# Performance work log

Hardware: AMD Instinct MI355X
Metric: run time of the kernel (lower is better)

The kernel has to match this reference:

```python
import jax, jax.numpy as jnp
import numpy as np

B, FRAMES, IMG, PATCH = 2, 4, 224, 16
D_MODEL, D_INNER, D_STATE, DT_RANK, DEPTH, D_CONV = 256, 512, 16, 16, 12, 4
NPATCH = (IMG // PATCH) ** 2  # 196


def setup_inputs() -> dict:
    keys = iter(jax.random.split(jax.random.key(0), 80))

    def n(shape, s=0.02):
        return jax.random.normal(next(keys), shape, dtype=jnp.float32) * s

    A_init = jnp.broadcast_to(jnp.log(jnp.arange(1, D_STATE + 1, dtype=jnp.float32)), (DEPTH, D_INNER, D_STATE))
    inp = {
        'x': jax.random.normal(next(keys), (B, 3, FRAMES, IMG, IMG), dtype=jnp.float32),
        'patch_w': n((D_MODEL, 3, 1, PATCH, PATCH)),
        'patch_b': jnp.zeros((D_MODEL,), jnp.float32),
        'pos_embed': n((1, NPATCH, D_MODEL)),
        'temp_pos': n((1, FRAMES, D_MODEL)),
        'in_proj_w': n((DEPTH, 2 * D_INNER, D_MODEL), D_MODEL ** -0.5),
        'convf_w': n((DEPTH, D_INNER, D_CONV), 0.3),
        'convf_b': jnp.zeros((DEPTH, D_INNER), jnp.float32),
        'xprojf_w': n((DEPTH, DT_RANK + 2 * D_STATE, D_INNER), D_INNER ** -0.5),
        'dtf_w': n((DEPTH, D_INNER, DT_RANK), DT_RANK ** -0.5),
        'dtf_b': jnp.full((DEPTH, D_INNER), -4.6, jnp.float32) + n((DEPTH, D_INNER), 0.1),
        'A_logf': A_init,
        'Dsf': jnp.ones((DEPTH, D_INNER), jnp.float32),
        'convb_w': n((DEPTH, D_INNER, D_CONV), 0.3),
        'convb_b': jnp.zeros((DEPTH, D_INNER), jnp.float32),
        'xprojb_w': n((DEPTH, DT_RANK + 2 * D_STATE, D_INNER), D_INNER ** -0.5),
        'dtb_w': n((DEPTH, D_INNER, DT_RANK), DT_RANK ** -0.5),
        'dtb_b': jnp.full((DEPTH, D_INNER), -4.6, jnp.float32) + n((DEPTH, D_INNER), 0.1),
        'A_logb': A_init,
        'Dsb': jnp.ones((DEPTH, D_INNER), jnp.float32),
        'out_proj_w': n((DEPTH, D_MODEL, D_INNER), D_INNER ** -0.5),
        'norm_w': jnp.ones((DEPTH, D_MODEL), jnp.float32),
        'normf_w': jnp.ones((D_MODEL,), jnp.float32),
        'bbox_w1': n((D_MODEL, D_MODEL), D_MODEL ** -0.5),
        'bbox_b1': jnp.zeros((D_MODEL,), jnp.float32),
        'bbox_w2': n((3, D_MODEL), D_MODEL ** -0.5),
        'bbox_b2': jnp.zeros((3,), jnp.float32),
        'pix_w1': n((4, D_MODEL, D_MODEL), D_MODEL ** -0.5),
        'pix_b1': jnp.zeros((4, D_MODEL), jnp.float32),
        'pix_w2': n((4, 2, D_MODEL), D_MODEL ** -0.5),
        'pix_b2': jnp.zeros((4, 2), jnp.float32),
    }
    return inp


def rmsnorm(x, w, eps=1e-5):
    x = x.astype(jnp.float32)
    return x * jax.lax.rsqrt(jnp.mean(x * x, axis=-1, keepdims=True) + eps) * w


def ssm_scan(u, dt, A, Bm, Cm):
    # u, dt: [B,L,di]; Bm, Cm: [B,L,st]; A: [di,st]
    def step(h, inp):
        dt_t, B_t, C_t, u_t = inp  # [B,di],[B,st],[B,st],[B,di]
        h = jnp.exp(dt_t[..., None] * A) * h + (dt_t * u_t)[..., None] * B_t[:, None, :]
        return h, jnp.einsum('bds,bs->bd', h, C_t)
    h0 = jnp.zeros((u.shape[0], u.shape[2], A.shape[1]), u.dtype)
    xs = (dt.swapaxes(0, 1), Bm.swapaxes(0, 1), Cm.swapaxes(0, 1), u.swapaxes(0, 1))
    _, ys = jax.lax.scan(step, h0, xs)
    return ys.swapaxes(0, 1)  # [B,L,di]


def mamba_dir(x, z, cw, cb, xpw, dtw, dtb, A_log, Ds):
    L = x.shape[1]
    xp = jnp.pad(x, ((0, 0), (D_CONV - 1, 0), (0, 0)))  # causal depthwise conv
    xc = cb + sum(xp[:, k:k + L, :] * cw[:, k] for k in range(D_CONV))
    xs = jax.nn.silu(xc)
    dbl = xs @ xpw.T  # [B,L,dt_rank+2*st]
    dt = jax.nn.softplus(dbl[..., :DT_RANK] @ dtw.T + dtb)
    Bm = dbl[..., DT_RANK:DT_RANK + D_STATE]
    Cm = dbl[..., DT_RANK + D_STATE:]
    y = ssm_scan(xs, dt, -jnp.exp(A_log), Bm, Cm) + Ds * xs
    return y * jax.nn.silu(z)


def _forward(x, patch_w, patch_b, pos_embed, temp_pos, in_proj_w, convf_w, convf_b, xprojf_w, dtf_w, dtf_b, A_logf, Dsf, convb_w, convb_b, xprojb_w, dtb_w, dtb_b, A_logb, Dsb, out_proj_w, norm_w, normf_w, bbox_w1, bbox_b1, bbox_w2, bbox_b2, pix_w1, pix_b1, pix_w2, pix_b2):
    feat = jax.lax.conv_general_dilated(x, patch_w, (1, PATCH, PATCH), 'VALID', dimension_numbers=('NCDHW', 'OIDHW', 'NCDHW'))
    feat = feat + patch_b[None, :, None, None, None]
    b, c, t, h, w = feat.shape
    np_ = h * w
    tok = feat.transpose(0, 2, 3, 4, 1).reshape(b * t, np_, c) + pos_embed
    tok = tok.reshape(b, t, np_, c).transpose(0, 2, 1, 3).reshape(b * np_, t, c) + temp_pos
    tok = tok.reshape(b, np_, t, c).transpose(0, 2, 1, 3).reshape(b, t * np_, c)
    hidden, residual = tok, None
    for i in range(DEPTH):
        residual = hidden if residual is None else hidden + residual  # fused add+norm (prenorm)
        hidden = rmsnorm(residual, norm_w[i])
        xz = hidden @ in_proj_w[i].T
        xi, zi = jnp.split(xz, 2, axis=-1)
        yf = mamba_dir(xi, zi, convf_w[i], convf_b[i], xprojf_w[i], dtf_w[i], dtf_b[i], A_logf[i], Dsf[i])
        yb = mamba_dir(xi[:, ::-1], zi[:, ::-1], convb_w[i], convb_b[i], xprojb_w[i], dtb_w[i], dtb_b[i], A_logb[i], Dsb[i])[:, ::-1]
        hidden = (yf + yb) @ out_proj_w[i].T
    residual = hidden + residual
    hidden = rmsnorm(residual, normf_w)
    fus = hidden[:, :5, :]  # [B,5,hidden_dim] fusion_output for DETR head
    bbox = jax.nn.relu(fus[:, 0] @ bbox_w1.T + bbox_b1) @ bbox_w2.T + bbox_b2  # [B,3]
    pix = jnp.stack([jax.nn.sigmoid(jax.nn.relu(fus[:, i + 1] @ pix_w1[i].T + pix_b1[i]) @ pix_w2[i].T + pix_b2[i]) for i in range(4)], axis=1)  # [B,4,2]
    return jnp.concatenate([bbox, pix.reshape(bbox.shape[0], 8)], axis=-1)  # [B,11]


def reference(x, patch_w, patch_b, pos_embed, temp_pos, in_proj_w, convf_w, convf_b, xprojf_w, dtf_w, dtf_b, A_logf, Dsf, convb_w, convb_b, xprojb_w, dtb_w, dtb_b, A_logb, Dsb, out_proj_w, norm_w, normf_w, bbox_w1, bbox_b1, bbox_w2, bbox_b2, pix_w1, pix_b1, pix_w2, pix_b2):
    return _forward(x, patch_w, patch_b, pos_embed, temp_pos, in_proj_w, convf_w, convf_b, xprojf_w, dtf_w, dtf_b, A_logf, Dsf, convb_w, convb_b, xprojb_w, dtb_w, dtb_b, A_logb, Dsb, out_proj_w, norm_w, normf_w, bbox_w1, bbox_b1, bbox_w2, bbox_b2, pix_w1, pix_b1, pix_w2, pix_b2)
```

## Files before the change

### kernel.cpp

```cpp
#include <hip/hip_runtime.h>
#include <hip/hip_bf16.h>
#include <cmath>

#define BB 2
#define TT 4
#define NPATCH 196
#define LL 784
#define CC 256
#define DI 512
#define NSTATE 16
#define DEPTH 12
#define NCHUNK 49
#define CLEN 16

typedef short short8 __attribute__((ext_vector_type(8)));
typedef float f32x4 __attribute__((ext_vector_type(4)));

__device__ __forceinline__ float sigmoidf_(float x){ return 1.f/(1.f+__expf(-x)); }
__device__ __forceinline__ float siluf_(float x){ return x/(1.f+__expf(-x)); }
__device__ __forceinline__ float softplusf_(float x){ return x > 20.f ? x : log1pf(__expf(x)); }
__device__ __forceinline__ unsigned short f2bf(float f){
  union { float f; unsigned int u; } v; v.f = f;
  unsigned int u = v.u;
  return (unsigned short)((u + 0x7FFFu + ((u>>16)&1u)) >> 16);
}

__global__ void k_cvt(const float* __restrict__ src, unsigned short* __restrict__ dst, int n4)
{
  int i = blockIdx.x*256 + threadIdx.x;
  if (i < n4) {
    float4 v = *(const float4*)(src + (size_t)i*4);
    unsigned short o[4] = { f2bf(v.x), f2bf(v.y), f2bf(v.z), f2bf(v.w) };
    *(uint2*)(dst + (size_t)i*4) = *(uint2*)o;
  }
}

__global__ void k_prep_xp(const float* __restrict__ xpf, const float* __restrict__ xpb,
                          unsigned short* __restrict__ Wxp)
{
  int blk = blockIdx.x;
  int r = blk & 63; int ld = blk >> 6;
  int layer = ld >> 1, dir = ld & 1;
  const float* src = dir ? xpb : xpf;
  for (int kk = threadIdx.x; kk < 512; kk += 256) {
    float v = (r < 48) ? src[((size_t)layer*48 + r)*512 + kk] : 0.f;
    Wxp[((size_t)blk)*512 + kk] = f2bf(v);
  }
}
__global__ void k_prep_dt(const float* __restrict__ dtwf, const float* __restrict__ dtwb,
                          unsigned short* __restrict__ Wdt)
{
  int idx = blockIdx.x*256 + threadIdx.x;
  int col = idx & 31; int rest = idx >> 5;
  int d = rest & 511; int ld = rest >> 9;
  int layer = ld >> 1, dir = ld & 1;
  const float* src = dir ? dtwb : dtwf;
  float v = (col < 16) ? src[((size_t)layer*512 + d)*16 + col] : 0.f;
  Wdt[idx] = f2bf(v);
}

__global__ void k_prebias(const float* __restrict__ pb, const float* __restrict__ pos,
                          const float* __restrict__ tpos, float* __restrict__ PB)
{
  int tp = blockIdx.x;
  int t = tp / NPATCH, p = tp - t*NPATCH;
  int c = threadIdx.x;
  PB[(size_t)tp*CC + c] = pb[c] + pos[(size_t)p*CC + c] + tpos[(size_t)t*CC + c];
}

__global__ void k_im2col(const float* __restrict__ x, unsigned short* __restrict__ XCol)
{
  int row = blockIdx.x, ci = blockIdx.y;
  int b = row / LL, rem = row - b*LL;
  int t = rem / NPATCH, p = rem - t*NPATCH;
  int ph = p / 14, pc = p - ph*14;
  int ii = threadIdx.x >> 4, jj = threadIdx.x & 15;
  float v = x[(((size_t)(b*3+ci)*TT + t)*224 + (ph*16+ii))*224 + (pc*16+jj)];
  XCol[(size_t)row*768 + ci*256 + threadIdx.x] = f2bf(v);
}

__global__ __launch_bounds__(256) void k_gemm_mfma(
    const unsigned short* __restrict__ Ab,
    const float* __restrict__ Af, const float* __restrict__ Af2,
    const unsigned short* __restrict__ Wb, float* __restrict__ Out,
    const float* __restrict__ bias, int M, int Nn, int K)
{
  __shared__ short As[64][40];
  __shared__ short Bs[64][40];
  int bm = blockIdx.x*64, bn = blockIdx.y*64;
  int tid = threadIdx.x;
  int wave = tid>>6, lane = tid&63;
  int wm = (wave>>1)*32, wn = (wave&1)*32;
  int quad = lane>>4, l16 = lane&15;
  f32x4 acc[2][2];
  #pragma unroll
  for (int i=0;i<2;i++)
    #pragma unroll
    for (int j=0;j<2;j++){ acc[i][j][0]=0.f; acc[i][j][1]=0.f; acc[i][j][2]=0.f; acc[i][j][3]=0.f; }
  int sr = tid>>2, sc = (tid&3)<<3;
  int gr = bm + sr;
  for (int k0 = 0; k0 < K; k0 += 32) {
    short8 av = {0,0,0,0,0,0,0,0};
    if (gr < M) {
      if (Ab) {
        av = *(const short8*)(Ab + (size_t)gr*K + k0 + sc);
      } else {
        float4 f0 = *(const float4*)(Af + (size_t)gr*K + k0 + sc);
        float4 f1 = *(const float4*)(Af + (size_t)gr*K + k0 + sc + 4);
        if (Af2) {
          float4 g0 = *(const float4*)(Af2 + (size_t)gr*K + k0 + sc);
          float4 g1 = *(const float4*)(Af2 + (size_t)gr*K + k0 + sc + 4);
          f0.x+=g0.x; f0.y+=g0.y; f0.z+=g0.z; f0.w+=g0.w;
          f1.x+=g1.x; f1.y+=g1.y; f1.z+=g1.z; f1.w+=g1.w;
        }
        av[0]=(short)f2bf(f0.x); av[1]=(short)f2bf(f0.y); av[2]=(short)f2bf(f0.z); av[3]=(short)f2bf(f0.w);
        av[4]=(short)f2bf(f1.x); av[5]=(short)f2bf(f1.y); av[6]=(short)f2bf(f1.z); av[7]=(short)f2bf(f1.w);
      }
    }
    *(short8*)&As[sr][sc] = av;
    short8 bv = *(const short8*)(Wb + (size_t)(bn+sr)*K + k0 + sc);
    *(short8*)&Bs[sr][sc] = bv;
    __syncthreads();
    short8 a0 = *(const short8*)&As[wm    +l16][quad<<3];
    short8 a1 = *(const short8*)&As[wm+16+l16][quad<<3];
    short8 b0 = *(const short8*)&Bs[wn    +l16][quad<<3];
    short8 b1 = *(const short8*)&Bs[wn+16+l16][quad<<3];
    acc[0][0] = __builtin_amdgcn_mfma_f32_16x16x32_bf16(a0,b0,acc[0][0],0,0,0);
    acc[0][1] = __builtin_amdgcn_mfma_f32_16x16x32_bf16(a0,b1,acc[0][1],0,0,0);
    acc[1][0] = __builtin_amdgcn_mfma_f32_16x16x32_bf16(a1,b0,acc[1][0],0,0,0);
    acc[1][1] = __builtin_amdgcn_mfma_f32_16x16x32_bf16(a1,b1,acc[1][1],0,0,0);
    __syncthreads();
  }
  #pragma unroll
  for (int i=0;i<2;i++){
    #pragma unroll
    for (int r=0;r<4;r++){
      int row = bm + wm + i*16 + quad*4 + r;
      if (row < M) {
        #pragma unroll
        for (int j=0;j<2;j++){
          int col = bn + wn + j*16 + l16;
          float vv = acc[i][j][r];
          if (bias) vv += bias[(size_t)(row % LL)*Nn + col];
          Out[(size_t)row*Nn + col] = vv;
        }
      }
    }
  }
}

__global__ __launch_bounds__(256) void k_gemm_xp(
    const unsigned short* __restrict__ XSb, const unsigned short* __restrict__ Wxp,
    float* __restrict__ DBL, unsigned short* __restrict__ DBLb)
{
  __shared__ short As[64][40];
  __shared__ short Bs[64][40];
  int z = blockIdx.z;
  int bm = blockIdx.x*64;
  const unsigned short* A = XSb + (size_t)z*2*LL*DI;
  const unsigned short* W = Wxp + (size_t)z*64*DI;
  int tid = threadIdx.x;
  int wave = tid>>6, lane = tid&63;
  int wm = (wave>>1)*32, wn = (wave&1)*32;
  int quad = lane>>4, l16 = lane&15;
  f32x4 acc[2][2];
  #pragma unroll
  for (int i=0;i<2;i++)
    #pragma unroll
    for (int j=0;j<2;j++){ acc[i][j][0]=0.f; acc[i][j][1]=0.f; acc[i][j][2]=0.f; acc[i][j][3]=0.f; }
  int sr = tid>>2, sc = (tid&3)<<3;
  int gr = bm + sr;
  for (int k0 = 0; k0 < DI; k0 += 32) {
    short8 av = {0,0,0,0,0,0,0,0};
    if (gr < 2*LL) av = *(const short8*)(A + (size_t)gr*DI + k0 + sc);
    *(short8*)&As[sr][sc] = av;
    *(short8*)&Bs[sr][sc] = *(const short8*)(W + (size_t)sr*DI + k0 + sc);
    __syncthreads();
    short8 a0 = *(const short8*)&As[wm    +l16][quad<<3];
    short8 a1 = *(const short8*)&As[wm+16+l16][quad<<3];
    short8 b0 = *(const short8*)&Bs[wn    +l16][quad<<3];
    short8 b1 = *(const short8*)&Bs[wn+16+l16][quad<<3];
    acc[0][0] = __builtin_amdgcn_mfma_f32_16x16x32_bf16(a0,b0,acc[0][0],0,0,0);
    acc[0][1] = __builtin_amdgcn_mfma_f32_16x16x32_bf16(a0,b1,acc[0][1],0,0,0);
    acc[1][0] = __builtin_amdgcn_mfma_f32_16x16x32_bf16(a1,b0,acc[1][0],0,0,0);
    acc[1][1] = __builtin_amdgcn_mfma_f32_16x16x32_bf16(a1,b1,acc[1][1],0,0,0);
    __syncthreads();
  }
  #pragma unroll
  for (int i=0;i<2;i++){
    #pragma unroll
    for (int r=0;r<4;r++){
      int row = bm + wm + i*16 + quad*4 + r;
      if (row < 2*LL) {
        size_t grow = (size_t)z*2*LL + row;
        #pragma unroll
        for (int j=0;j<2;j++){
          int col = wn + j*16 + l16;
          float vv = acc[i][j][r];
          DBL[grow*64 + col] = vv;
          if (col < 32) DBLb[grow*32 + col] = (col < 16) ? f2bf(vv) : (unsigned short)0;
        }
      }
    }
  }
}

__global__ __launch_bounds__(256) void k_gemm_dt(
    const unsigned short* __restrict__ DBLb, const unsigned short* __restrict__ Wdt,
    const float* __restrict__ dtbf, const float* __restrict__ dtbb,
    float* __restrict__ DTs)
{
  __shared__ short As[64][40];
  __shared__ short Bs[64][40];
  int z = blockIdx.z;
  int bm = blockIdx.x*64, bn = blockIdx.y*64;
  const unsigned short* A = DBLb + (size_t)z*2*LL*32;
  const unsigned short* W = Wdt + (size_t)z*DI*32;
  const float* dtb = z ? dtbb : dtbf;
  int tid = threadIdx.x;
  int wave = tid>>6, lane = tid&63;
  int wm = (wave>>1)*32, wn = (wave&1)*32;
  int quad = lane>>4, l16 = lane&15;
  f32x4 acc[2][2];
  #pragma unroll
  for (int i=0;i<2;i++)
    #pragma unroll
    for (int j=0;j<2;j++){ acc[i][j][0]=0.f; acc[i][j][1]=0.f; acc[i][j][2]=0.f; acc[i][j][3]=0.f; }
  int sr = tid>>2, sc = (tid&3)<<3;
  int gr = bm + sr;
  {
    short8 av = {0,0,0,0,0,0,0,0};
    if (gr < 2*LL) av = *(const short8*)(A + (size_t)gr*32 + sc);
    *(short8*)&As[sr][sc] = av;
    *(short8*)&Bs[sr][sc] = *(const short8*)(W + (size_t)(bn+sr)*32 + sc);
    __syncthreads();
    short8 a0 = *(const short8*)&As[wm    +l16][quad<<3];
    short8 a1 = *(const short8*)&As[wm+16+l16][quad<<3];
    short8 b0 = *(const short8*)&Bs[wn    +l16][quad<<3];
    short8 b1 = *(const short8*)&Bs[wn+16+l16][quad<<3];
    acc[0][0] = __builtin_amdgcn_mfma_f32_16x16x32_bf16(a0,b0,acc[0][0],0,0,0);
    acc[0][1] = __builtin_amdgcn_mfma_f32_16x16x32_bf16(a0,b1,acc[0][1],0,0,0);
    acc[1][0] = __builtin_amdgcn_mfma_f32_16x16x32_bf16(a1,b0,acc[1][0],0,0,0);
    acc[1][1] = __builtin_amdgcn_mfma_f32_16x16x32_bf16(a1,b1,acc[1][1],0,0,0);
  }
  #pragma unroll
  for (int i=0;i<2;i++){
    #pragma unroll
    for (int r=0;r<4;r++){
      int row = bm + wm + i*16 + quad*4 + r;
      if (row < 2*LL) {
        size_t grow = (size_t)z*2*LL + row;
        #pragma unroll
        for (int j=0;j<2;j++){
          int col = bn + wn + j*16 + l16;
          DTs[grow*DI + col] = softplusf_(acc[i][j][r] + dtb[col]);
        }
      }
    }
  }
}

__global__ void k_conv_silu(const float* __restrict__ XZ,
    const float* __restrict__ cwf, const float* __restrict__ cbf,
    const float* __restrict__ cwb, const float* __restrict__ cbb,
    float* __restrict__ XSf, unsigned short* __restrict__ XSb)
{
  int dir = blockIdx.z;
  int row = blockIdx.x;
  int b = row / LL, tau = row - b*LL;
  const float* cw = dir ? cwb : cwf;
  const float* cb = dir ? cbb : cbf;
  int d = threadIdx.x;
  float4 w4 = *(const float4*)(cw + (size_t)d*4);
  float acc = cb[d];
  const float wr[4] = {w4.x, w4.y, w4.z, w4.w};
  #pragma unroll
  for (int k=0;k<4;k++){
    int tt = tau - 3 + k;
    if (tt >= 0) {
      int torig = dir ? (LL-1-tt) : tt;
      acc = fmaf(XZ[((size_t)b*LL + torig)*1024 + d], wr[k], acc);
    }
  }
  float xs = siluf_(acc);
  size_t rowbase = (size_t)(dir*BB + b)*LL + tau;
  XSf[rowbase*DI + d] = xs;
  XSb[rowbase*DI + d] = f2bf(xs);
}

__global__ void k_res_rms(const float* __restrict__ Hin, float* __restrict__ R,
                          unsigned short* __restrict__ Nout, const float* __restrict__ w, int first)
{
  int row = blockIdx.x, c = threadIdx.x;
  size_t idx = (size_t)row*CC + c;
  float h = Hin[idx];
  float r = first ? h : (h + R[idx]);
  R[idx] = r;
  float v = r*r;
  #pragma unroll
  for (int m=1;m<64;m<<=1) v += __shfl_xor(v,m);
  __shared__ float sred[4];
  if ((c & 63)==0) sred[c>>6]=v;
  __syncthreads();
  float tot = sred[0]+sred[1]+sred[2]+sred[3];
  float sc = rsqrtf(tot*(1.f/CC) + 1e-5f);
  Nout[idx] = f2bf(r*sc*w[c]);
}

__global__ void k_scan1(const float* __restrict__ XS, const float* __restrict__ DBL,
                        const float* __restrict__ DTs,
                        const float* __restrict__ Alf, const float* __restrict__ Alb,
                        float* __restrict__ Pb, float* __restrict__ Hcb)
{
  int chunk = blockIdx.x;
  int d = blockIdx.y*256 + threadIdx.x;
  int dirb = blockIdx.z;
  int dir = dirb >> 1;
  const float* Al = dir ? Alb : Alf;
  float a2[NSTATE];
  {
    const float4* ar = (const float4*)(Al + (size_t)d*NSTATE);
    #pragma unroll
    for (int q=0;q<4;q++){
      float4 v = ar[q];
      a2[q*4+0] = -__expf(v.x)*1.44269504f;
      a2[q*4+1] = -__expf(v.y)*1.44269504f;
      a2[q*4+2] = -__expf(v.z)*1.44269504f;
      a2[q*4+3] = -__expf(v.w)*1.44269504f;
    }
  }
  __shared__ float Bl[CLEN][NSTATE];
  {
    int t = threadIdx.x >> 4, s = threadIdx.x & 15;
    size_t row = ((size_t)dirb*LL + chunk*CLEN + t)*64;
    Bl[t][s] = DBL[row + 16 + s];
  }
  __syncthreads();
  size_t base = (size_t)dirb*LL*DI;
  const float* xs  = XS  + base + (size_t)chunk*CLEN*DI + d;
  const float* dtp = DTs + base + (size_t)chunk*CLEN*DI + d;
  float P[NSTATE], h[NSTATE];
  #pragma unroll
  for (int s=0;s<NSTATE;s++){ P[s]=1.f; h[s]=0.f; }
  for (int i = 0; i < CLEN; ++i) {
    float dt = dtp[(size_t)i*DI];
    float u  = xs[(size_t)i*DI];
    float du = dt*u;
    #pragma unroll
    for (int s=0;s<NSTATE;s++){
      float e = exp2f(dt*a2[s]);
      P[s] *= e;
      h[s] = fmaf(e, h[s], du*Bl[i][s]);
    }
  }
  size_t ob = ((size_t)dirb*NCHUNK + chunk)*NSTATE*DI + d;
  #pragma unroll
  for (int s=0;s<NSTATE;s++){
    Pb [ob + (size_t)s*DI] = P[s];
    Hcb[ob + (size_t)s*DI] = h[s];
  }
}

__global__ void k_scan2(const float* __restrict__ Pb, float* __restrict__ Hcb)
{
  int i = blockIdx.x*256 + threadIdx.x;
  int dirb = blockIdx.y;
  float h = 0.f;
  for (int c = 0; c < NCHUNK; ++c) {
    size_t idx = ((size_t)dirb*NCHUNK + c)*NSTATE*DI + i;
    float p = Pb[idx], hl = Hcb[idx];
    Hcb[idx] = h;
    h = fmaf(p, h, hl);
  }
}

__global__ void k_scan3(const float* __restrict__ XS, const float* __restrict__ DBL,
                        const float* __restrict__ DTs, const float* __restrict__ XZ,
                        const float* __restrict__ Alf, const float* __restrict__ Alb,
                        const float* __restrict__ Dsfp, const float* __restrict__ Dsbp,
                        const float* __restrict__ Hcb, float* __restrict__ Y)
{
  int chunk = blockIdx.x;
  int d = blockIdx.y*256 + threadIdx.x;
  int dirb = blockIdx.z;
  int dir = dirb >> 1, b = dirb & 1;
  const float* Al = dir ? Alb : Alf;
  float a2[NSTATE];
  {
    const float4* ar = (const float4*)(Al + (size_t)d*NSTATE);
    #pragma unroll
    for (int q=0;q<4;q++){
      float4 v = ar[q];
      a2[q*4+0] = -__expf(v.x)*1.44269504f;
      a2[q*4+1] = -__expf(v.y)*1.44269504f;
      a2[q*4+2] = -__expf(v.z)*1.44269504f;
      a2[q*4+3] = -__expf(v.w)*1.44269504f;
    }
  }
  __shared__ float BCl[CLEN][32];
  {
    for (int idx = threadIdx.x; idx < CLEN*32; idx += 256) {
      int t = idx >> 5, j = idx & 31;
      size_t row = ((size_t)dirb*LL + chunk*CLEN + t)*64;
      BCl[t][j] = DBL[row + 16 + j];
    }
  }
  __syncthreads();
  float h[NSTATE];
  size_t ob = ((size_t)dirb*NCHUNK + chunk)*NSTATE*DI + d;
  #pragma unroll
  for (int s=0;s<NSTATE;s++) h[s] = Hcb[ob + (size_t)s*DI];
  float Dsv = (dir ? Dsbp : Dsfp)[d];
  size_t base = (size_t)dirb*LL*DI;
  const float* xs  = XS  + base + (size_t)chunk*CLEN*DI + d;
  const float* dtp = DTs + base + (size_t)chunk*CLEN*DI + d;
  const float* zpb = XZ + (size_t)b*LL*1024 + 512 + d;
  float* y = Y + base + d;
  for (int i = 0; i < CLEN; ++i) {
    int tau = chunk*CLEN + i;
    float dt = dtp[(size_t)i*DI];
    float u  = xs[(size_t)i*DI];
    float du = dt*u;
    float yacc = 0.f;
    #pragma unroll
    for (int s=0;s<NSTATE;s++){
      float e = exp2f(dt*a2[s]);
      h[s] = fmaf(e, h[s], du*BCl[i][s]);
      yacc = fmaf(h[s], BCl[i][16+s], yacc);
    }
    int torig = dir ? (LL-1-tau) : tau;
    float zv = zpb[(size_t)torig*1024];
    y[(size_t)torig*DI] = (yacc + Dsv*u) * siluf_(zv);
  }
}

__global__ void k_head(const float* __restrict__ H, const float* __restrict__ R,
                       const float* __restrict__ nw,
                       const float* __restrict__ bw1, const float* __restrict__ bb1,
                       const float* __restrict__ bw2, const float* __restrict__ bb2,
                       const float* __restrict__ pw1, const float* __restrict__ pb1,
                       const float* __restrict__ pw2, const float* __restrict__ pb2,
                       float* __restrict__ out)
{
  int b = blockIdx.x / 5, j = blockIdx.x % 5;
  int c = threadIdx.x;
  __shared__ float fus[CC], h1[CC];
  __shared__ float sred[4];
  size_t idx = ((size_t)b*LL + j)*CC + c;
  float r = H[idx] + R[idx];
  float v = r*r;
  #pragma unroll
  for (int m=1;m<64;m<<=1) v += __shfl_xor(v,m);
  if ((c&63)==0) sred[c>>6]=v;
  __syncthreads();
  float tot = sred[0]+sred[1]+sred[2]+sred[3];
  fus[c] = r * rsqrtf(tot*(1.f/CC)+1e-5f) * nw[c];
  __syncthreads();
  const float* W1 = (j==0) ? bw1 : (pw1 + (size_t)(j-1)*CC*CC);
  const float* B1 = (j==0) ? bb1 : (pb1 + (j-1)*CC);
  float a = B1[c];
  for (int k=0;k<CC;k++) a = fmaf(fus[k], W1[(size_t)c*CC+k], a);
  h1[c] = fmaxf(a, 0.f);
  __syncthreads();
  if (j==0) {
    if (c < 3) {
      float o = bb2[c];
      for (int k=0;k<CC;k++) o = fmaf(h1[k], bw2[c*CC+k], o);
      out[b*11 + c] = o;
    }
  } else {
    if (c < 2) {
      const float* W2 = pw2 + (size_t)((j-1)*2 + c)*CC;
      float o = pb2[(j-1)*2 + c];
      for (int k=0;k<CC;k++) o = fmaf(h1[k], W2[k], o);
      out[b*11 + 3 + (j-1)*2 + c] = sigmoidf_(o);
    }
  }
}

extern "C" void kernel_launch(void* const* d_in, const int* in_sizes, int n_in,
                              void* d_out, int out_size, void* d_ws, size_t ws_size,
                              hipStream_t stream)
{
  const float* x        = (const float*)d_in[0];
  const float* patch_w  = (const float*)d_in[1];
  const float* patch_b  = (const float*)d_in[2];
  const float* pos      = (const float*)d_in[3];
  const float* tpos     = (const float*)d_in[4];
  const float* in_proj  = (const float*)d_in[5];
  const float* convf_w  = (const float*)d_in[6];
  const float* convf_b  = (const float*)d_in[7];
  const float* xprojf_w = (const float*)d_in[8];
  const float* dtf_w    = (const float*)d_in[9];
  const float* dtf_b    = (const float*)d_in[10];
  const float* A_logf   = (const float*)d_in[11];
  const float* Dsf      = (const float*)d_in[12];
  const float* convb_w  = (const float*)d_in[13];
  const float* convb_b  = (const float*)d_in[14];
  const float* xprojb_w = (const float*)d_in[15];
  const float* dtb_w    = (const float*)d_in[16];
  const float* dtb_b    = (const float*)d_in[17];
  const float* A_logb   = (const float*)d_in[18];
  const float* Dsb      = (const float*)d_in[19];
  const float* out_proj = (const float*)d_in[20];
  const float* norm_w   = (const float*)d_in[21];
  const float* normf_w  = (const float*)d_in[22];
  const float* bbox_w1  = (const float*)d_in[23];
  const float* bbox_b1  = (const float*)d_in[24];
  const float* bbox_w2  = (const float*)d_in[25];
  const float* bbox_b2  = (const float*)d_in[26];
  const float* pix_w1   = (const float*)d_in[27];
  const float* pix_b1   = (const float*)d_in[28];
  const float* pix_w2   = (const float*)d_in[29];
  const float* pix_b2   = (const float*)d_in[30];
  float* out = (float*)d_out;

  float* ws = (float*)d_ws;
  const size_t nTok = (size_t)BB*LL;
  float* H   = ws;                 ws += nTok*CC;
  float* R   = ws;                 ws += nTok*CC;
  float* XZ  = ws;                 ws += nTok*1024;
  float* XSf = ws;                 ws += 2*nTok*DI;
  float* DBL = ws;                 ws += 2*nTok*64;
  float* DTs = ws;                 ws += 2*nTok*DI;
  float* Y   = ws;                 ws += 2*nTok*DI;
  float* Pb  = ws;                 ws += (size_t)4*NCHUNK*NSTATE*DI;
  float* Hcb = ws;                 ws += (size_t)4*NCHUNK*NSTATE*DI;
  float* PB  = ws;                 ws += (size_t)LL*CC;
  unsigned short* WinB  = (unsigned short*)ws;  ws += (size_t)DEPTH*1024*CC/2;
  unsigned short* WoutB = (unsigned short*)ws;  ws += (size_t)DEPTH*CC*DI/2;
  unsigned short* WpB   = (unsigned short*)ws;  ws += (size_t)CC*768/2;
  unsigned short* XCol  = (unsigned short*)ws;  ws += nTok*768/2;
  unsigned short* NrmB  = (unsigned short*)ws;  ws += nTok*CC/2;
  unsigned short* XSb   = (unsigned short*)ws;  ws += 2*nTok*DI/2;
  unsigned short* DBLb  = (unsigned short*)ws;  ws += 2*nTok*32/2;
  unsigned short* Wxp   = (unsigned short*)ws;  ws += (size_t)DEPTH*2*64*DI/2;
  unsigned short* Wdt   = (unsigned short*)ws;  ws += (size_t)DEPTH*2*DI*32/2;
  (void)ws_size; (void)in_sizes; (void)n_in; (void)out_size;

  {
    int n4 = DEPTH*1024*CC/4;
    k_cvt<<<dim3((n4+255)/256), 256, 0, stream>>>(in_proj, WinB, n4);
    n4 = DEPTH*CC*DI/4;
    k_cvt<<<dim3((n4+255)/256), 256, 0, stream>>>(out_proj, WoutB, n4);
    n4 = CC*768/4;
    k_cvt<<<dim3((n4+255)/256), 256, 0, stream>>>(patch_w, WpB, n4);
    k_prep_xp<<<dim3(DEPTH*2*64), 256, 0, stream>>>(xprojf_w, xprojb_w, Wxp);
    k_prep_dt<<<dim3(DEPTH*2*DI*32/256), 256, 0, stream>>>(dtf_w, dtb_w, Wdt);
  }
  k_prebias<<<dim3(LL), CC, 0, stream>>>(patch_b, pos, tpos, PB);
  k_im2col<<<dim3((unsigned)nTok, 3), 256, 0, stream>>>(x, XCol);
  k_gemm_mfma<<<dim3(25, 4), 256, 0, stream>>>(XCol, nullptr, nullptr, WpB, H, PB,
                                               (int)nTok, CC, 768);

  for (int i = 0; i < DEPTH; ++i) {
    k_res_rms<<<dim3((unsigned)nTok), 256, 0, stream>>>(H, R, NrmB, norm_w + i*CC, i==0 ? 1 : 0);
    k_gemm_mfma<<<dim3(25, 16), 256, 0, stream>>>(NrmB, nullptr, nullptr,
        WinB + (size_t)i*1024*CC, XZ, nullptr, (int)nTok, 1024, CC);
    k_conv_silu<<<dim3((unsigned)nTok, 1, 2), DI, 0, stream>>>(XZ,
        convf_w + (size_t)i*DI*4, convf_b + (size_t)i*DI,
        convb_w + (size_t)i*DI*4, convb_b + (size_t)i*DI, XSf, XSb);
    k_gemm_xp<<<dim3(25, 1, 2), 256, 0, stream>>>(XSb,
        Wxp + (size_t)i*2*64*DI, DBL, DBLb);
    k_gemm_dt<<<dim3(25, 8, 2), 256, 0, stream>>>(DBLb,
        Wdt + (size_t)i*2*DI*32, dtf_b + (size_t)i*DI, dtb_b + (size_t)i*DI, DTs);
    k_scan1<<<dim3(NCHUNK, 2, 4), 256, 0, stream>>>(XSf, DBL, DTs,
        A_logf + (size_t)i*DI*NSTATE, A_logb + (size_t)i*DI*NSTATE, Pb, Hcb);
    k_scan2<<<dim3(32, 4), 256, 0, stream>>>(Pb, Hcb);
    k_scan3<<<dim3(NCHUNK, 2, 4), 256, 0, stream>>>(XSf, DBL, DTs, XZ,
        A_logf + (size_t)i*DI*NSTATE, A_logb + (size_t)i*DI*NSTATE,
        Dsf + (size_t)i*DI, Dsb + (size_t)i*DI, Hcb, Y);
    k_gemm_mfma<<<dim3(25, 4), 256, 0, stream>>>(nullptr, Y, Y + nTok*DI,
        WoutB + (size_t)i*CC*DI, H, nullptr, (int)nTok, CC, DI);
  }
  k_head<<<dim3(10), 256, 0, stream>>>(H, R, normf_w, bbox_w1, bbox_b1, bbox_w2, bbox_b2,
                                       pix_w1, pix_b1, pix_w2, pix_b2, out);
}
```

Measured before the change: 1.347 ms.

## Fuse depthwise conv+SiLU, x_proj GEMM and dt_proj GEMM into one kernel

Merges the causal conv/SiLU kernel, the x_proj MFMA GEMM and the dt_proj GEMM into a single kernel per layer. Conv output is computed directly into the GEMM's shared-memory A tile, and the x_proj result is staged in shared memory as the dt_proj A operand, removing the DBLb buffer and two launches. The trade-off is only 50 blocks doing all the work, including the previously 400-block dt GEMM and 1568x2-block conv, which reduces parallelism on a large GPU.

```diff
diff --git a/kernel.cpp b/kernel.cpp
--- a/kernel.cpp
+++ b/kernel.cpp
@@ -149,16 +149,26 @@
   }
 }
 
-__global__ __launch_bounds__(256) void k_gemm_xp(
-    const unsigned short* __restrict__ XSb, const unsigned short* __restrict__ Wxp,
-    float* __restrict__ DBL, unsigned short* __restrict__ DBLb)
-{
+__global__ __launch_bounds__(256) void k_conv_xp_dt(
+    const float* __restrict__ XZ,
+    const float* __restrict__ cwf, const float* __restrict__ cbf,
+    const float* __restrict__ cwb, const float* __restrict__ cbb,
+    const unsigned short* __restrict__ Wxp,
+    const unsigned short* __restrict__ Wdt,
+    const float* __restrict__ dtbf, const float* __restrict__ dtbb,
+    float* __restrict__ XSf, unsigned short* __restrict__ XSb,
+    float* __restrict__ DBL, float* __restrict__ DTs)
+{
+  int z = blockIdx.z;
+  int bm = blockIdx.x*64;
+  const float* cw  = z ? cwb : cwf;
+  const float* cb  = z ? cbb : cbf;
+  const float* dtb = z ? dtbb : dtbf;
+  const unsigned short* Wx = Wxp + (size_t)z*64*DI;
+  const unsigned short* Wd = Wdt + (size_t)z*DI*32;
   __shared__ short As[64][40];
   __shared__ short Bs[64][40];
-  int z = blockIdx.z;
-  int bm = blockIdx.x*64;
-  const unsigned short* A = XSb + (size_t)z*2*LL*DI;
-  const unsigned short* W = Wxp + (size_t)z*64*DI;
+  __shared__ short Adt[64][40];
   int tid = threadIdx.x;
   int wave = tid>>6, lane = tid&63;
   int wm = (wave>>1)*32, wn = (wave&1)*32;
@@ -170,11 +180,49 @@
     for (int j=0;j<2;j++){ acc[i][j][0]=0.f; acc[i][j][1]=0.f; acc[i][j][2]=0.f; acc[i][j][3]=0.f; }
   int sr = tid>>2, sc = (tid&3)<<3;
   int gr = bm + sr;
+  bool live = gr < 2*LL;
+  int b = gr / LL, tau = gr - b*LL;
+  size_t xsrow = ((size_t)z*2*LL + gr)*DI;
+
   for (int k0 = 0; k0 < DI; k0 += 32) {
     short8 av = {0,0,0,0,0,0,0,0};
-    if (gr < 2*LL) av = *(const short8*)(A + (size_t)gr*DI + k0 + sc);
+    if (live) {
+      float c0[8];
+      {
+        float4 b0_ = *(const float4*)(cb + k0 + sc);
+        float4 b1_ = *(const float4*)(cb + k0 + sc + 4);
+        c0[0]=b0_.x; c0[1]=b0_.y; c0[2]=b0_.z; c0[3]=b0_.w;
+        c0[4]=b1_.x; c0[5]=b1_.y; c0[6]=b1_.z; c0[7]=b1_.w;
+      }
+      float w[8][4];
+      #pragma unroll
+      for (int j=0;j<8;j++){
+        float4 wv = *(const float4*)(cw + (size_t)(k0+sc+j)*4);
+        w[j][0]=wv.x; w[j][1]=wv.y; w[j][2]=wv.z; w[j][3]=wv.w;
+      }
+      #pragma unroll
+      for (int k=0;k<4;k++){
+        int tt = tau - 3 + k;
+        if (tt >= 0) {
+          int torig = z ? (LL-1-tt) : tt;
+          const float* p = XZ + ((size_t)(b*LL + torig))*1024 + k0 + sc;
+          float4 v0 = *(const float4*)p;
+          float4 v1 = *(const float4*)(p+4);
+          c0[0]=fmaf(v0.x,w[0][k],c0[0]); c0[1]=fmaf(v0.y,w[1][k],c0[1]);
+          c0[2]=fmaf(v0.z,w[2][k],c0[2]); c0[3]=fmaf(v0.w,w[3][k],c0[3]);
+          c0[4]=fmaf(v1.x,w[4][k],c0[4]); c0[5]=fmaf(v1.y,w[5][k],c0[5]);
+          c0[6]=fmaf(v1.z,w[6][k],c0[6]); c0[7]=fmaf(v1.w,w[7][k],c0[7]);
+        }
+      }
+      float xsv[8];
+      #pragma unroll
+      for (int j=0;j<8;j++){ xsv[j] = siluf_(c0[j]); av[j] = (short)f2bf(xsv[j]); }
+      *(float4*)(XSf + xsrow + k0 + sc)     = make_float4(xsv[0],xsv[1],xsv[2],xsv[3]);
+      *(float4*)(XSf + xsrow + k0 + sc + 4) = make_float4(xsv[4],xsv[5],xsv[6],xsv[7]);
+      *(short8*)(XSb + xsrow + k0 + sc) = av;
+    }
     *(short8*)&As[sr][sc] = av;
-    *(short8*)&Bs[sr][sc] = *(const short8*)(W + (size_t)sr*DI + k0 + sc);
+    *(short8*)&Bs[sr][sc] = *(const short8*)(Wx + (size_t)sr*DI + k0 + sc);
     __syncthreads();
     short8 a0 = *(const short8*)&As[wm    +l16][quad<<3];
     short8 a1 = *(const short8*)&As[wm+16+l16][quad<<3];
@@ -186,11 +234,18 @@
     acc[1][1] = __builtin_amdgcn_mfma_f32_16x16x32_bf16(a1,b1,acc[1][1],0,0,0);
     __syncthreads();
   }
+
+  {
+    short8 zz = {0,0,0,0,0,0,0,0};
+    *(short8*)&Adt[sr][sc] = zz;
+  }
+  __syncthreads();
   #pragma unroll
   for (int i=0;i<2;i++){
     #pragma unroll
     for (int r=0;r<4;r++){
-      int row = bm + wm + i*16 + quad*4 + r;
+      int lrow = wm + i*16 + quad*4 + r;
+      int row = bm + lrow;
       if (row < 2*LL) {
         size_t grow = (size_t)z*2*LL + row;
         #pragma unroll
@@ -198,94 +253,46 @@
           int col = wn + j*16 + l16;
           float vv = acc[i][j][r];
           DBL[grow*64 + col] = vv;
-          if (col < 32) DBLb[grow*32 + col] = (col < 16) ? f2bf(vv) : (unsigned short)0;
+          if (col < 16) Adt[lrow][col] = (short)f2bf(vv);
         }
       }
     }
   }
-}
-
-__global__ __launch_bounds__(256) void k_gemm_dt(
-    const unsigned short* __restrict__ DBLb, const unsigned short* __restrict__ Wdt,
-    const float* __restrict__ dtbf, const float* __restrict__ dtbb,
-    float* __restrict__ DTs)
-{
-  __shared__ short As[64][40];
-  __shared__ short Bs[64][40];
-  int z = blockIdx.z;
-  int bm = blockIdx.x*64, bn = blockIdx.y*64;
-  const unsigned short* A = DBLb + (size_t)z*2*LL*32;
-  const unsigned short* W = Wdt + (size_t)z*DI*32;
-  const float* dtb = z ? dtbb : dtbf;
-  int tid = threadIdx.x;
-  int wave = tid>>6, lane = tid&63;
-  int wm = (wave>>1)*32, wn = (wave&1)*32;
-  int quad = lane>>4, l16 = lane&15;
-  f32x4 acc[2][2];
-  #pragma unroll
-  for (int i=0;i<2;i++)
-    #pragma unroll
-    for (int j=0;j<2;j++){ acc[i][j][0]=0.f; acc[i][j][1]=0.f; acc[i][j][2]=0.f; acc[i][j][3]=0.f; }
-  int sr = tid>>2, sc = (tid&3)<<3;
-  int gr = bm + sr;
-  {
-    short8 av = {0,0,0,0,0,0,0,0};
-    if (gr < 2*LL) av = *(const short8*)(A + (size_t)gr*32 + sc);
-    *(short8*)&As[sr][sc] = av;
-    *(short8*)&Bs[sr][sc] = *(const short8*)(W + (size_t)(bn+sr)*32 + sc);
+  __syncthreads();
+
+  short8 a0 = *(const short8*)&Adt[wm    +l16][quad<<3];
+  short8 a1 = *(const short8*)&Adt[wm+16+l16][quad<<3];
+  for (int nb = 0; nb < 8; ++nb) {
+    *(short8*)&Bs[sr][sc & 31] = *(const short8*)(Wd + (size_t)(nb*64 + sr)*32 + (sc & 31));
     __syncthreads();
-    short8 a0 = *(const short8*)&As[wm    +l16][quad<<3];
-    short8 a1 = *(const short8*)&As[wm+16+l16][quad<<3];
+    f32x4 dacc[2][2];
+    #pragma unroll
+    for (int i=0;i<2;i++)
+      #pragma unroll
+      for (int j=0;j<2;j++){ dacc[i][j][0]=0.f; dacc[i][j][1]=0.f; dacc[i][j][2]=0.f; dacc[i][j][3]=0.f; }
     short8 b0 = *(const short8*)&Bs[wn    +l16][quad<<3];
     short8 b1 = *(const short8*)&Bs[wn+16+l16][quad<<3];
-    acc[0][0] = __builtin_amdgcn_mfma_f32_16x16x32_bf16(a0,b0,acc[0][0],0,0,0);
-    acc[0][1] = __builtin_amdgcn_mfma_f32_16x16x32_bf16(a0,b1,acc[0][1],0,0,0);
-    acc[1][0] = __builtin_amdgcn_mfma_f32_16x16x32_bf16(a1,b0,acc[1][0],0,0,0);
-    acc[1][1] = __builtin_amdgcn_mfma_f32_16x16x32_bf16(a1,b1,acc[1][1],0,0,0);
-  }
-  #pragma unroll
-  for (int i=0;i<2;i++){
-    #pragma unroll
-    for (int r=0;r<4;r++){
-      int row = bm + wm + i*16 + quad*4 + r;
-      if (row < 2*LL) {
-        size_t grow = (size_t)z*2*LL + row;
-        #pragma unroll
-        for (int j=0;j<2;j++){
-          int col = bn + wn + j*16 + l16;
-          DTs[grow*DI + col] = softplusf_(acc[i][j][r] + dtb[col]);
+    dacc[0][0] = __builtin_amdgcn_mfma_f32_16x16x32_bf16(a0,b0,dacc[0][0],0,0,0);
+    dacc[0][1] = __builtin_amdgcn_mfma_f32_16x16x32_bf16(a0,b1,dacc[0][1],0,0,0);
+    dacc[1][0] = __builtin_amdgcn_mfma_f32_16x16x32_bf16(a1,b0,dacc[1][0],0,0,0);
+    dacc[1][1] = __builtin_amdgcn_mfma_f32_16x16x32_bf16(a1,b1,dacc[1][1],0,0,0);
+    #pragma unroll
+    for (int i=0;i<2;i++){
+      #pragma unroll
+      for (int r=0;r<4;r++){
+        int row = bm + wm + i*16 + quad*4 + r;
+        if (row < 2*LL) {
+          size_t grow = (size_t)z*2*LL + row;
+          #pragma unroll
+          for (int j=0;j<2;j++){
+            int colg = nb*64 + wn + j*16 + l16;
+            DTs[grow*DI + colg] = softplusf_(dacc[i][j][r] + dtb[colg]);
+          }
         }
       }
     }
-  }
-}
-
-__global__ void k_conv_silu(const float* __restrict__ XZ,
-    const float* __restrict__ cwf, const float* __restrict__ cbf,
-    const float* __restrict__ cwb, const float* __restrict__ cbb,
-    float* __restrict__ XSf, unsigned short* __restrict__ XSb)
-{
-  int dir = blockIdx.z;
-  int row = blockIdx.x;
-  int b = row / LL, tau = row - b*LL;
-  const float* cw = dir ? cwb : cwf;
-  const float* cb = dir ? cbb : cbf;
-  int d = threadIdx.x;
-  float4 w4 = *(const float4*)(cw + (size_t)d*4);
-  float acc = cb[d];
-  const float wr[4] = {w4.x, w4.y, w4.z, w4.w};
-  #pragma unroll
-  for (int k=0;k<4;k++){
-    int tt = tau - 3 + k;
-    if (tt >= 0) {
-      int torig = dir ? (LL-1-tt) : tt;
-      acc = fmaf(XZ[((size_t)b*LL + torig)*1024 + d], wr[k], acc);
-    }
-  }
-  float xs = siluf_(acc);
-  size_t rowbase = (size_t)(dir*BB + b)*LL + tau;
-  XSf[rowbase*DI + d] = xs;
-  XSb[rowbase*DI + d] = f2bf(xs);
+    __syncthreads();
+  }
 }
 
 __global__ void k_res_rms(const float* __restrict__ Hin, float* __restrict__ R,
@@ -533,7 +540,6 @@
   unsigned short* XCol  = (unsigned short*)ws;  ws += nTok*768/2;
   unsigned short* NrmB  = (unsigned short*)ws;  ws += nTok*CC/2;
   unsigned short* XSb   = (unsigned short*)ws;  ws += 2*nTok*DI/2;
-  unsigned short* DBLb  = (unsigned short*)ws;  ws += 2*nTok*32/2;
   unsigned short* Wxp   = (unsigned short*)ws;  ws += (size_t)DEPTH*2*64*DI/2;
   unsigned short* Wdt   = (unsigned short*)ws;  ws += (size_t)DEPTH*2*DI*32/2;
   (void)ws_size; (void)in_sizes; (void)n_in; (void)out_size;
@@ -557,13 +563,12 @@
     k_res_rms<<<dim3((unsigned)nTok), 256, 0, stream>>>(H, R, NrmB, norm_w + i*CC, i==0 ? 1 : 0);
     k_gemm_mfma<<<dim3(25, 16), 256, 0, stream>>>(NrmB, nullptr, nullptr,
         WinB + (size_t)i*1024*CC, XZ, nullptr, (int)nTok, 1024, CC);
-    k_conv_silu<<<dim3((unsigned)nTok, 1, 2), DI, 0, stream>>>(XZ,
+    k_conv_xp_dt<<<dim3(25, 1, 2), 256, 0, stream>>>(XZ,
         convf_w + (size_t)i*DI*4, convf_b + (size_t)i*DI,
-        convb_w + (size_t)i*DI*4, convb_b + (size_t)i*DI, XSf, XSb);
-    k_gemm_xp<<<dim3(25, 1, 2), 256, 0, stream>>>(XSb,
-        Wxp + (size_t)i*2*64*DI, DBL, DBLb);
-    k_gemm_dt<<<dim3(25, 8, 2), 256, 0, stream>>>(DBLb,
-        Wdt + (size_t)i*2*DI*32, dtf_b + (size_t)i*DI, dtb_b + (size_t)i*DI, DTs);
+        convb_w + (size_t)i*DI*4, convb_b + (size_t)i*DI,
+        Wxp + (size_t)i*2*64*DI, Wdt + (size_t)i*2*DI*32,
+        dtf_b + (size_t)i*DI, dtb_b + (size_t)i*DI,
+        XSf, XSb, DBL, DTs);
     k_scan1<<<dim3(NCHUNK, 2, 4), 256, 0, stream>>>(XSf, DBL, DTs,
         A_logf + (size_t)i*DI*NSTATE, A_logb + (size_t)i*DI*NSTATE, Pb, Hcb);
     k_scan2<<<dim3(32, 4), 256, 0, stream>>>(Pb, Hcb);
```

Measured after the change: 3.684 ms. +173.5%, slower.
